# Performance work log

Hardware: AMD Instinct MI355X
Metric: run time of the kernel (lower is better)

Reference implementation:

```python
import jax, jax.numpy as jnp
import numpy as np

SEQ_LEN = 4096
INPUT_SIZE = 1024
OUTPUT_SIZE = 1024


def _xavier(key, shape):
    n = shape[0]
    lim = 1.0 / (n ** 0.5)
    return jax.random.uniform(key, shape, minval=-lim, maxval=lim, dtype=jnp.float32)


def setup_inputs() -> dict:
    key = jax.random.key(0)
    kx, kk, kv, kq = jax.random.split(key, 4)
    X = jax.random.normal(kx, (SEQ_LEN, INPUT_SIZE), dtype=jnp.float32)
    Wk = _xavier(kk, (INPUT_SIZE, OUTPUT_SIZE))
    Wv = _xavier(kv, (INPUT_SIZE, OUTPUT_SIZE))
    Wq = _xavier(kq, (INPUT_SIZE, OUTPUT_SIZE))
    return {"X": X, "Wk": Wk, "Wv": Wv, "Wq": Wq}


def reference(X, Wk, Wv, Wq):
    # Faithful to original: scores = K @ Q^T (note K first, no 1/sqrt(d) scaling)
    K = X @ Wk  # (S, D)
    V = X @ Wv  # (S, D)
    Q = X @ Wq  # (S, D)
    scores = jnp.einsum('sd,td->st', K, Q)  # (S, S) == K @ Q^T
    attn = jax.nn.softmax(scores, axis=-1) @ V  # (S, D)
    return attn
```

## Files before the change

### kernel.cpp

```cpp
#include <hip/hip_runtime.h>
#include <hip/hip_fp16.h>
#include <cstdint>

#define SEQ 4096
#define DIM 1024

typedef _Float16 f16x8 __attribute__((ext_vector_type(8)));
typedef float f32x4 __attribute__((ext_vector_type(4)));
typedef __attribute__((address_space(1))) void as1_void;
typedef __attribute__((address_space(3))) void as3_void;

__device__ __forceinline__ ushort f2h(float f) {
  _Float16 h = (_Float16)f;
  return __builtin_bit_cast(ushort, h);
}

__global__ void convert_x_kernel(const float* __restrict__ X, ushort* __restrict__ Xh, int n4) {
  int i = blockIdx.x * blockDim.x + threadIdx.x;
  if (i >= n4) return;
  float4 v = reinterpret_cast<const float4*>(X)[i];
  ushort4 o = { f2h(v.x), f2h(v.y), f2h(v.z), f2h(v.w) };
  reinterpret_cast<ushort4*>(Xh)[i] = o;
}

__global__ void convert_w_kernel(const float* __restrict__ Wk, const float* __restrict__ Wv,
                                 const float* __restrict__ Wq, ushort* __restrict__ Wt) {
  __shared__ float tile[32][33];
  int z = blockIdx.z;
  const float* W = (z == 0) ? Wk : (z == 1) ? Wv : Wq;
  int n0 = blockIdx.x * 32, k0 = blockIdx.y * 32;
  int tx = threadIdx.x, ty = threadIdx.y;
#pragma unroll
  for (int r = 0; r < 4; r++) {
    int k = ty + r * 8;
    tile[k][tx] = W[(size_t)(k0 + k) * DIM + n0 + tx];
  }
  __syncthreads();
  ushort* out = Wt + (size_t)z * DIM * DIM;
#pragma unroll
  for (int r = 0; r < 4; r++) {
    int n = ty + r * 8;
    out[(size_t)(n0 + n) * DIM + k0 + tx] = f2h(tile[tx][n]);
  }
}

template <bool F16_OUT>
__device__ __forceinline__ void gemm_tile(const ushort* __restrict__ A,
                                          const ushort* __restrict__ B,
                                          void* __restrict__ C,
                                          int N, int K, int m0, int n0,
                                          int kt0, int ktend) {
  constexpr int BK = 64;
  __shared__ __align__(16) ushort As[128 * BK];
  __shared__ __align__(16) ushort Bs[128 * BK];
  const int tid = threadIdx.x;
  const int wave = tid >> 6, lane = tid & 63;
  const int lane15 = lane & 15, quad = lane >> 4;
  const int wm = (wave & 1) * 64, wn = (wave >> 1) * 64;

  const int srow = tid >> 3;
  const int sce = (((tid & 7) ^ ((tid >> 3) & 7)) * 8);
  const int rs = lane15 & 7;

  f32x4 acc[4][4];
#pragma unroll
  for (int i = 0; i < 4; i++)
#pragma unroll
    for (int j = 0; j < 4; j++) {
      f32x4 z = {0.f, 0.f, 0.f, 0.f};
      acc[i][j] = z;
    }

  for (int kt = kt0; kt < ktend; kt += BK) {
    __syncthreads();
#pragma unroll
    for (int q = 0; q < 4; q++) {
      const ushort* ga = A + (size_t)(m0 + srow + q * 32) * K + kt + sce;
      __builtin_amdgcn_global_load_lds((const as1_void*)ga,
                                       (as3_void*)&As[wave * 512 + q * 2048], 16, 0, 0);
    }
#pragma unroll
    for (int q = 0; q < 4; q++) {
      const ushort* gb = B + (size_t)(n0 + srow + q * 32) * K + kt + sce;
      __builtin_amdgcn_global_load_lds((const as1_void*)gb,
                                       (as3_void*)&Bs[wave * 512 + q * 2048], 16, 0, 0);
    }
    __syncthreads();
#pragma unroll
    for (int ks = 0; ks < 2; ks++) {
      f16x8 af[4], bfr[4];
#pragma unroll
      for (int i = 0; i < 4; i++)
        af[i] = *reinterpret_cast<const f16x8*>(
            &As[(wm + i * 16 + lane15) * BK + (((ks * 4 + quad) ^ rs) * 8)]);
#pragma unroll
      for (int j = 0; j < 4; j++)
        bfr[j] = *reinterpret_cast<const f16x8*>(
            &Bs[(wn + j * 16 + lane15) * BK + (((ks * 4 + quad) ^ rs) * 8)]);
#pragma unroll
      for (int i = 0; i < 4; i++)
#pragma unroll
        for (int j = 0; j < 4; j++)
          acc[i][j] = __builtin_amdgcn_mfma_f32_16x16x32_f16(af[i], bfr[j], acc[i][j], 0, 0, 0);
    }
  }

  const int rbase = m0 + wm + quad * 4;
  const int cbase = n0 + wn + lane15;
#pragma unroll
  for (int i = 0; i < 4; i++)
#pragma unroll
    for (int j = 0; j < 4; j++)
#pragma unroll
      for (int r = 0; r < 4; r++) {
        int row = rbase + i * 16 + r;
        int col = cbase + j * 16;
        if (F16_OUT)
          reinterpret_cast<ushort*>(C)[(size_t)row * N + col] = f2h(acc[i][j][r]);
        else
          reinterpret_cast<float*>(C)[(size_t)row * N + col] = acc[i][j][r];
      }
}

__global__ __launch_bounds__(256) void proj_kernel(const ushort* __restrict__ Xh,
                                                   const ushort* __restrict__ Wt,
                                                   ushort* __restrict__ Kh,
                                                   ushort* __restrict__ Qh,
                                                   ushort* __restrict__ Vt) {
  const int z = blockIdx.z;
  const ushort* A;
  const ushort* B;
  ushort* C;
  int N, m0, n0;
  if (z < 2) {
    A = Xh;
    B = Wt + (size_t)(z == 0 ? 0 : 2) * DIM * DIM;
    C = (z == 0) ? Kh : Qh;
    N = DIM;
    m0 = (blockIdx.x >> 3) * 128;
    n0 = (blockIdx.x & 7) * 128;
  } else {
    A = Wt + (size_t)DIM * DIM;
    B = Xh;
    C = Vt;
    N = SEQ;
    m0 = (blockIdx.x >> 5) * 128;
    n0 = (blockIdx.x & 31) * 128;
  }
  gemm_tile<true>(A, B, C, N, DIM, m0, n0, 0, DIM);
}

__global__ __launch_bounds__(256) void score_kernel(const ushort* __restrict__ Kh,
                                                    const ushort* __restrict__ Qh,
                                                    ushort* __restrict__ S) {
  const int f = blockIdx.x;
  const int xcd = f & 7;
  const int r = f >> 3;
  const int t = xcd * 128 + r;
  const int st = t >> 6, within = t & 63;
  const int sx = within & 7, sy = within >> 3;
  const int tx = (st & 3) * 8 + sx;
  const int ty = (st >> 2) * 8 + sy;
  gemm_tile<true>(Kh, Qh, S, SEQ, DIM, ty * 128, tx * 128, 0, DIM);
}

__global__ __launch_bounds__(256) void out_splitk_kernel(const ushort* __restrict__ P,
                                                         const ushort* __restrict__ Vt,
                                                         ushort* __restrict__ Part) {
  const int f = blockIdx.x;
  const int z = f >> 8;
  const int q = f & 255;
  const int xcd = q & 7;
  const int r = q >> 3;
  const int t = xcd * 32 + r;
  const int tx = t & 7, ty = t >> 3;
  ushort* C = Part + (size_t)z * SEQ * DIM;
  gemm_tile<true>(P, Vt, C, DIM, SEQ, ty * 128, tx * 128,
                  z * (SEQ / 4), (z + 1) * (SEQ / 4));
}

__global__ void reduce4_kernel(const ushort* __restrict__ Part, float* __restrict__ out, int n8) {
  int i = blockIdx.x * blockDim.x + threadIdx.x;
  if (i >= n8) return;
  const f16x8* p0 = reinterpret_cast<const f16x8*>(Part);
  const f16x8* p1 = p0 + n8;
  const f16x8* p2 = p1 + n8;
  const f16x8* p3 = p2 + n8;
  f16x8 a = p0[i], b = p1[i], c = p2[i], d = p3[i];
  float4 lo, hi;
  lo.x = (float)a[0] + (float)b[0] + (float)c[0] + (float)d[0];
  lo.y = (float)a[1] + (float)b[1] + (float)c[1] + (float)d[1];
  lo.z = (float)a[2] + (float)b[2] + (float)c[2] + (float)d[2];
  lo.w = (float)a[3] + (float)b[3] + (float)c[3] + (float)d[3];
  hi.x = (float)a[4] + (float)b[4] + (float)c[4] + (float)d[4];
  hi.y = (float)a[5] + (float)b[5] + (float)c[5] + (float)d[5];
  hi.z = (float)a[6] + (float)b[6] + (float)c[6] + (float)d[6];
  hi.w = (float)a[7] + (float)b[7] + (float)c[7] + (float)d[7];
  reinterpret_cast<float4*>(out)[i * 2] = lo;
  reinterpret_cast<float4*>(out)[i * 2 + 1] = hi;
}

__global__ __launch_bounds__(256) void softmax_kernel(const ushort* __restrict__ S,
                                                      ushort* __restrict__ P) {
  const int row = blockIdx.x;
  const ushort* s = S + (size_t)row * SEQ;
  const int tid = threadIdx.x;
  const int wave = tid >> 6, lane = tid & 63;
  __shared__ float red[4];
  float v[16];
#pragma unroll
  for (int i = 0; i < 2; i++) {
    f16x8 h = reinterpret_cast<const f16x8*>(s)[tid + i * 256];
#pragma unroll
    for (int j = 0; j < 8; j++) v[i * 8 + j] = (float)h[j];
  }
  float m = v[0];
#pragma unroll
  for (int j = 1; j < 16; j++) m = fmaxf(m, v[j]);
#pragma unroll
  for (int o = 32; o > 0; o >>= 1) m = fmaxf(m, __shfl_xor(m, o, 64));
  if (lane == 0) red[wave] = m;
  __syncthreads();
  m = fmaxf(fmaxf(red[0], red[1]), fmaxf(red[2], red[3]));
  __syncthreads();
  float sum = 0.f;
#pragma unroll
  for (int j = 0; j < 16; j++) {
    v[j] = __expf(v[j] - m);
    sum += v[j];
  }
#pragma unroll
  for (int o = 32; o > 0; o >>= 1) sum += __shfl_xor(sum, o, 64);
  if (lane == 0) red[wave] = sum;
  __syncthreads();
  sum = red[0] + red[1] + red[2] + red[3];
  float inv = 1.0f / sum;
  ushort* p = P + (size_t)row * SEQ;
#pragma unroll
  for (int i = 0; i < 2; i++) {
    ushort4 o4a = { f2h(v[i * 8 + 0] * inv), f2h(v[i * 8 + 1] * inv),
                    f2h(v[i * 8 + 2] * inv), f2h(v[i * 8 + 3] * inv) };
    ushort4 o4b = { f2h(v[i * 8 + 4] * inv), f2h(v[i * 8 + 5] * inv),
                    f2h(v[i * 8 + 6] * inv), f2h(v[i * 8 + 7] * inv) };
    reinterpret_cast<ushort4*>(p)[(tid + i * 256) * 2] = o4a;
    reinterpret_cast<ushort4*>(p)[(tid + i * 256) * 2 + 1] = o4b;
  }
}

extern "C" void kernel_launch(void* const* d_in, const int* in_sizes, int n_in,
                              void* d_out, int out_size, void* d_ws, size_t ws_size,
                              hipStream_t stream) {
  const float* X = (const float*)d_in[0];
  const float* Wk = (const float*)d_in[1];
  const float* Wv = (const float*)d_in[2];
  const float* Wq = (const float*)d_in[3];

  char* ws = (char*)d_ws;
  size_t off = 0;
  ushort* Xh = (ushort*)(ws + off); off += (size_t)SEQ * DIM * 2;
  ushort* Wt = (ushort*)(ws + off); off += (size_t)3 * DIM * DIM * 2;
  ushort* Kh = (ushort*)(ws + off); off += (size_t)SEQ * DIM * 2;
  ushort* Qh = (ushort*)(ws + off); off += (size_t)SEQ * DIM * 2;
  ushort* Vt = (ushort*)(ws + off); off += (size_t)SEQ * DIM * 2;
  ushort* S = (ushort*)(ws + off);  off += (size_t)SEQ * SEQ * 2;
  ushort* P = (ushort*)(ws + off);  off += (size_t)SEQ * SEQ * 2;

  ushort* Part = S;

  convert_x_kernel<<<SEQ * DIM / 4 / 256, 256, 0, stream>>>(X, Xh, SEQ * DIM / 4);
  convert_w_kernel<<<dim3(DIM / 32, DIM / 32, 3), dim3(32, 8), 0, stream>>>(Wk, Wv, Wq, Wt);

  proj_kernel<<<dim3(256, 1, 3), 256, 0, stream>>>(Xh, Wt, Kh, Qh, Vt);
  score_kernel<<<1024, 256, 0, stream>>>(Kh, Qh, S);
  softmax_kernel<<<SEQ, 256, 0, stream>>>(S, P);
  out_splitk_kernel<<<1024, 256, 0, stream>>>(P, Vt, Part);
  reduce4_kernel<<<SEQ * DIM / 8 / 256, 256, 0, stream>>>(Part, (float*)d_out, SEQ * DIM / 8);
}
```

Measured before the change: 224.2 us.

## Use 32x32x16 MFMA tiles, fuse conversion kernels, wave-per-row softmax

The shared GEMM tile routine now issues 32x32x16 f16 MFMA instructions on 2x2 accumulator blocks per wave instead of 4x4 blocks of 16x16x32. This cuts LDS fragment loads per MFMA, and the LDS swizzle is adjusted to match. The X and weight conversions are merged into one launch. Softmax now gives each wave a full row and reduces with shuffles only, dropping the shared-memory reductions and barriers. The trade-off is higher register pressure from 64 values per lane in softmax and a different epilogue store pattern.

```diff
diff --git a/kernel.cpp b/kernel.cpp
--- a/kernel.cpp
+++ b/kernel.cpp
@@ -6,7 +6,7 @@
 #define DIM 1024
 
 typedef _Float16 f16x8 __attribute__((ext_vector_type(8)));
-typedef float f32x4 __attribute__((ext_vector_type(4)));
+typedef float f32x16 __attribute__((ext_vector_type(16)));
 typedef __attribute__((address_space(1))) void as1_void;
 typedef __attribute__((address_space(3))) void as3_void;
 
@@ -15,21 +15,26 @@
   return __builtin_bit_cast(ushort, h);
 }
 
-__global__ void convert_x_kernel(const float* __restrict__ X, ushort* __restrict__ Xh, int n4) {
-  int i = blockIdx.x * blockDim.x + threadIdx.x;
-  if (i >= n4) return;
-  float4 v = reinterpret_cast<const float4*>(X)[i];
-  ushort4 o = { f2h(v.x), f2h(v.y), f2h(v.z), f2h(v.w) };
-  reinterpret_cast<ushort4*>(Xh)[i] = o;
-}
-
-__global__ void convert_w_kernel(const float* __restrict__ Wk, const float* __restrict__ Wv,
-                                 const float* __restrict__ Wq, ushort* __restrict__ Wt) {
+__global__ void convert_all_kernel(const float* __restrict__ X, const float* __restrict__ Wk,
+                                   const float* __restrict__ Wv, const float* __restrict__ Wq,
+                                   ushort* __restrict__ Xh, ushort* __restrict__ Wt) {
+  const int z = blockIdx.z;
+  const int tx = threadIdx.x, ty = threadIdx.y;
+  if (z == 3) {
+    const int bid = blockIdx.y * 32 + blockIdx.x;
+    const int t = ty * 32 + tx;
+#pragma unroll
+    for (int k = 0; k < 4; k++) {
+      int i = bid * 1024 + k * 256 + t;
+      float4 v = reinterpret_cast<const float4*>(X)[i];
+      ushort4 o = { f2h(v.x), f2h(v.y), f2h(v.z), f2h(v.w) };
+      reinterpret_cast<ushort4*>(Xh)[i] = o;
+    }
+    return;
+  }
   __shared__ float tile[32][33];
-  int z = blockIdx.z;
   const float* W = (z == 0) ? Wk : (z == 1) ? Wv : Wq;
   int n0 = blockIdx.x * 32, k0 = blockIdx.y * 32;
-  int tx = threadIdx.x, ty = threadIdx.y;
 #pragma unroll
   for (int r = 0; r < 4; r++) {
     int k = ty + r * 8;
@@ -55,21 +60,21 @@
   __shared__ __align__(16) ushort Bs[128 * BK];
   const int tid = threadIdx.x;
   const int wave = tid >> 6, lane = tid & 63;
-  const int lane15 = lane & 15, quad = lane >> 4;
+  const int l31 = lane & 31, khalf = lane >> 5;
   const int wm = (wave & 1) * 64, wn = (wave >> 1) * 64;
 
   const int srow = tid >> 3;
-  const int sce = (((tid & 7) ^ ((tid >> 3) & 7)) * 8);
-  const int rs = lane15 & 7;
-
-  f32x4 acc[4][4];
-#pragma unroll
-  for (int i = 0; i < 4; i++)
-#pragma unroll
-    for (int j = 0; j < 4; j++) {
-      f32x4 z = {0.f, 0.f, 0.f, 0.f};
-      acc[i][j] = z;
-    }
+  const int skey = ((srow & 7) ^ ((srow >> 3) & 3));
+  const int sce = (((tid & 7) ^ skey) * 8);
+  const int rk = (l31 & 7) ^ ((l31 >> 3) & 3);
+
+  f32x16 acc[2][2];
+#pragma unroll
+  for (int i = 0; i < 2; i++)
+#pragma unroll
+    for (int j = 0; j < 2; j++)
+#pragma unroll
+      for (int r = 0; r < 16; r++) acc[i][j][r] = 0.f;
 
   for (int kt = kt0; kt < ktend; kt += BK) {
     __syncthreads();
@@ -87,34 +92,33 @@
     }
     __syncthreads();
 #pragma unroll
-    for (int ks = 0; ks < 2; ks++) {
-      f16x8 af[4], bfr[4];
-#pragma unroll
-      for (int i = 0; i < 4; i++)
+    for (int ks = 0; ks < 4; ks++) {
+      f16x8 af[2], bfr[2];
+      const int ck = (ks * 2 + khalf);
+#pragma unroll
+      for (int i = 0; i < 2; i++)
         af[i] = *reinterpret_cast<const f16x8*>(
-            &As[(wm + i * 16 + lane15) * BK + (((ks * 4 + quad) ^ rs) * 8)]);
-#pragma unroll
-      for (int j = 0; j < 4; j++)
+            &As[(wm + i * 32 + l31) * BK + ((ck ^ rk) * 8)]);
+#pragma unroll
+      for (int j = 0; j < 2; j++)
         bfr[j] = *reinterpret_cast<const f16x8*>(
-            &Bs[(wn + j * 16 + lane15) * BK + (((ks * 4 + quad) ^ rs) * 8)]);
-#pragma unroll
-      for (int i = 0; i < 4; i++)
-#pragma unroll
-        for (int j = 0; j < 4; j++)
-          acc[i][j] = __builtin_amdgcn_mfma_f32_16x16x32_f16(af[i], bfr[j], acc[i][j], 0, 0, 0);
-    }
-  }
-
-  const int rbase = m0 + wm + quad * 4;
-  const int cbase = n0 + wn + lane15;
-#pragma unroll
-  for (int i = 0; i < 4; i++)
-#pragma unroll
-    for (int j = 0; j < 4; j++)
-#pragma unroll
-      for (int r = 0; r < 4; r++) {
-        int row = rbase + i * 16 + r;
-        int col = cbase + j * 16;
+            &Bs[(wn + j * 32 + l31) * BK + ((ck ^ rk) * 8)]);
+#pragma unroll
+      for (int i = 0; i < 2; i++)
+#pragma unroll
+        for (int j = 0; j < 2; j++)
+          acc[i][j] = __builtin_amdgcn_mfma_f32_32x32x16_f16(af[i], bfr[j], acc[i][j], 0, 0, 0);
+    }
+  }
+
+#pragma unroll
+  for (int i = 0; i < 2; i++)
+#pragma unroll
+    for (int j = 0; j < 2; j++)
+#pragma unroll
+      for (int r = 0; r < 16; r++) {
+        int row = m0 + wm + i * 32 + (r & 3) + 8 * (r >> 2) + 4 * khalf;
+        int col = n0 + wn + j * 32 + l31;
         if (F16_OUT)
           reinterpret_cast<ushort*>(C)[(size_t)row * N + col] = f2h(acc[i][j][r]);
         else
@@ -202,48 +206,37 @@
 
 __global__ __launch_bounds__(256) void softmax_kernel(const ushort* __restrict__ S,
                                                       ushort* __restrict__ P) {
-  const int row = blockIdx.x;
+  const int wave = threadIdx.x >> 6, lane = threadIdx.x & 63;
+  const int row = blockIdx.x * 4 + wave;
   const ushort* s = S + (size_t)row * SEQ;
-  const int tid = threadIdx.x;
-  const int wave = tid >> 6, lane = tid & 63;
-  __shared__ float red[4];
-  float v[16];
-#pragma unroll
-  for (int i = 0; i < 2; i++) {
-    f16x8 h = reinterpret_cast<const f16x8*>(s)[tid + i * 256];
+  float v[64];
+#pragma unroll
+  for (int i = 0; i < 8; i++) {
+    f16x8 h = reinterpret_cast<const f16x8*>(s)[i * 64 + lane];
 #pragma unroll
     for (int j = 0; j < 8; j++) v[i * 8 + j] = (float)h[j];
   }
   float m = v[0];
 #pragma unroll
-  for (int j = 1; j < 16; j++) m = fmaxf(m, v[j]);
+  for (int j = 1; j < 64; j++) m = fmaxf(m, v[j]);
 #pragma unroll
   for (int o = 32; o > 0; o >>= 1) m = fmaxf(m, __shfl_xor(m, o, 64));
-  if (lane == 0) red[wave] = m;
-  __syncthreads();
-  m = fmaxf(fmaxf(red[0], red[1]), fmaxf(red[2], red[3]));
-  __syncthreads();
   float sum = 0.f;
 #pragma unroll
-  for (int j = 0; j < 16; j++) {
+  for (int j = 0; j < 64; j++) {
     v[j] = __expf(v[j] - m);
     sum += v[j];
   }
 #pragma unroll
   for (int o = 32; o > 0; o >>= 1) sum += __shfl_xor(sum, o, 64);
-  if (lane == 0) red[wave] = sum;
-  __syncthreads();
-  sum = red[0] + red[1] + red[2] + red[3];
   float inv = 1.0f / sum;
   ushort* p = P + (size_t)row * SEQ;
 #pragma unroll
-  for (int i = 0; i < 2; i++) {
-    ushort4 o4a = { f2h(v[i * 8 + 0] * inv), f2h(v[i * 8 + 1] * inv),
-                    f2h(v[i * 8 + 2] * inv), f2h(v[i * 8 + 3] * inv) };
-    ushort4 o4b = { f2h(v[i * 8 + 4] * inv), f2h(v[i * 8 + 5] * inv),
-                    f2h(v[i * 8 + 6] * inv), f2h(v[i * 8 + 7] * inv) };
-    reinterpret_cast<ushort4*>(p)[(tid + i * 256) * 2] = o4a;
-    reinterpret_cast<ushort4*>(p)[(tid + i * 256) * 2 + 1] = o4b;
+  for (int i = 0; i < 8; i++) {
+    f16x8 h;
+#pragma unroll
+    for (int j = 0; j < 8; j++) h[j] = (_Float16)(v[i * 8 + j] * inv);
+    reinterpret_cast<f16x8*>(p)[i * 64 + lane] = h;
   }
 }
 
@@ -267,12 +260,10 @@
 
   ushort* Part = S;
 
-  convert_x_kernel<<<SEQ * DIM / 4 / 256, 256, 0, stream>>>(X, Xh, SEQ * DIM / 4);
-  convert_w_kernel<<<dim3(DIM / 32, DIM / 32, 3), dim3(32, 8), 0, stream>>>(Wk, Wv, Wq, Wt);
-
+  convert_all_kernel<<<dim3(32, 32, 4), dim3(32, 8), 0, stream>>>(X, Wk, Wv, Wq, Xh, Wt);
   proj_kernel<<<dim3(256, 1, 3), 256, 0, stream>>>(Xh, Wt, Kh, Qh, Vt);
   score_kernel<<<1024, 256, 0, stream>>>(Kh, Qh, S);
-  softmax_kernel<<<SEQ, 256, 0, stream>>>(S, P);
+  softmax_kernel<<<1024, 256, 0, stream>>>(S, P);
   out_splitk_kernel<<<1024, 256, 0, stream>>>(P, Vt, Part);
   reduce4_kernel<<<SEQ * DIM / 8 / 256, 256, 0, stream>>>(Part, (float*)d_out, SEQ * DIM / 8);
 }
```

Measured after the change: 211.0 us. 5.9% less time.
